# Kernel tuning notes

Hardware: AMD Instinct MI355X
Metric: run time of the kernel (lower is better)

The kernel has to match this reference:

```python
import jax, jax.numpy as jnp
import numpy as np

B, Nq, Nk, R = 4, 1024, 1024, 256
NH, DK, DV = 8, 64, 64


def setup_inputs() -> dict:
    key = jax.random.key(0)
    ks = jax.random.split(key, 16)
    mk = lambda k, shape, s=1.0: jax.random.normal(k, shape, dtype=jnp.float32) * s
    inp = {
        'Q_real': mk(ks[0], (B, Nq, R)), 'Q_imag': mk(ks[1], (B, Nq, R)),
        'K_real': mk(ks[2], (B, Nk, R)), 'K_imag': mk(ks[3], (B, Nk, R)),
        'V_real': mk(ks[4], (B, Nk, R)), 'V_imag': mk(ks[5], (B, Nk, R)),
        'WQ_r': mk(ks[6], (NH * DK, R), 0.02), 'WQ_i': mk(ks[7], (NH * DK, R), 0.02),
        'WK_r': mk(ks[8], (NH * DK, R), 0.02), 'WK_i': mk(ks[9], (NH * DK, R), 0.02),
        'WV_r': mk(ks[10], (NH * DV, R), 0.02), 'WV_i': mk(ks[11], (NH * DV, R), 0.02),
        'WO_r': mk(ks[12], (R, NH * DV), 0.02), 'WO_i': mk(ks[13], (R, NH * DV), 0.02),
        'mask': jax.random.randint(ks[14], (B, Nk), 0, 2).astype(bool),
    }
    return inp


def _complex_linear(x, w_r, w_i):
    # x: complex [..., in]; weights real [out, in]. Same math as 4 real matmuls.
    w = (w_r + 1j * w_i).astype(jnp.complex64)
    return x @ w.T


def reference(Q_real, Q_imag, K_real, K_imag, V_real, V_imag,
              WQ_r, WQ_i, WK_r, WK_i, WV_r, WV_i, WO_r, WO_i, mask):
    Q = (Q_real + 1j * Q_imag).astype(jnp.complex64)
    K = (K_real + 1j * K_imag).astype(jnp.complex64)
    V = (V_real + 1j * V_imag).astype(jnp.complex64)

    Qp = _complex_linear(Q, WQ_r, WQ_i).reshape(B, Nq, NH, DK).transpose(0, 2, 1, 3)
    Kp = _complex_linear(K, WK_r, WK_i).reshape(B, Nk, NH, DK).transpose(0, 2, 1, 3)
    Vp = _complex_linear(V, WV_r, WV_i).reshape(B, Nk, NH, DV).transpose(0, 2, 1, 3)

    # complex scores [B, NH, Nq, Nk]; conj on K matches torch .conj().transpose
    scores = jnp.einsum('bhqd,bhkd->bhqk', Qp, jnp.conj(Kp)) / jnp.sqrt(jnp.float32(DK))
    scores_abs = jnp.abs(scores)

    m = mask[:, None, None, :]                    # [B,1,1,Nk]
    valid = jnp.any(mask, axis=-1)[:, None, None, None]  # [B,1,1,1] valid query rows
    masked = jnp.where(m, scores_abs, -jnp.inf)
    # avoid all -inf rows feeding softmax (those rows are zeroed afterwards)
    safe = jnp.where(valid, masked, 0.0)
    w = jax.nn.softmax(safe, axis=-1)
    w = jnp.where(valid, w, 0.0)

    attn = jnp.einsum('bhqk,bhkd->bhqd', w.astype(Vp.dtype), Vp)
    attn = attn.transpose(0, 2, 1, 3).reshape(B, Nq, NH * DV)
    return _complex_linear(attn, WO_r, WO_i)
```

## Files before the change

kernel.cpp:

```cpp
#include <hip/hip_runtime.h>
#include <hip/hip_bf16.h>

#define NBATCH 4
#define NSEQ   1024
#define RD     256
#define NHEAD  8
#define HD     64
#define NHD    512

typedef __attribute__((ext_vector_type(8))) short  short8;
typedef __attribute__((ext_vector_type(4))) short  short4v;
typedef __attribute__((ext_vector_type(4))) float  float4v;

#define MFMA16(a,b,c) __builtin_amdgcn_mfma_f32_16x16x32_bf16(a,b,c,0,0,0)

typedef const void __attribute__((address_space(1)))* gas_t;
typedef void __attribute__((address_space(3)))* las_t;
#define GLOAD16(g, l) __builtin_amdgcn_global_load_lds((gas_t)(g), (las_t)(l), 16, 0, 0)

static __device__ __forceinline__ short f2b(float f) {
    __hip_bfloat16 h = __float2bfloat16(f);
    union { __hip_bfloat16 h; short s; } u; u.h = h;
    return u.s;
}
static __device__ __forceinline__ void st4(short* dst, float4v v) {
    short4v p;
    p[0] = f2b(v[0]); p[1] = f2b(v[1]);
    p[2] = f2b(v[2]); p[3] = f2b(v[3]);
    *(short4v*)dst = p;
}

struct ConvArgs { const float* src[15]; short* dst[15]; int n4[15]; };

__global__ __launch_bounds__(256) void convert_bf16(ConvArgs ca)
{
    const int a = blockIdx.y;
    if (a == 14) {
        if (blockIdx.x != 0) return;
        __shared__ int isByteLayout;
        const int t = threadIdx.x;
        if (t == 0) isByteLayout = 0;
        __syncthreads();
        const int* mi = (const int*)ca.src[14];
        #pragma unroll
        for (int j = 0; j < 4; j++) {
            int v = mi[t*4 + j];
            if (v & ~1) isByteLayout = 1;
        }
        __syncthreads();
        const unsigned char* mb = (const unsigned char*)ca.src[14];
        unsigned char mv[16];
        int lc = 0;
        if (isByteLayout) {
            #pragma unroll
            for (int j = 0; j < 16; j++) { mv[j] = mb[t*16 + j] ? 1 : 0; lc += mv[j]; }
        } else {
            #pragma unroll
            for (int j = 0; j < 16; j++) { mv[j] = mi[t*16 + j] ? 1 : 0; lc += mv[j]; }
        }
        const int lane = t & 63, b = t >> 6;
        int sum = lc;
        #pragma unroll
        for (int d = 1; d < 64; d <<= 1) {
            int o = __shfl_up(sum, d, 64);
            if (lane >= d) sum += o;
        }
        int p = sum - lc;
        unsigned short* idxOut = (unsigned short*)ca.dst[14];
        int* cntOut = (int*)(idxOut + 4096);
        unsigned short* ib = idxOut + b*1024;
        #pragma unroll
        for (int j = 0; j < 16; j++)
            if (mv[j]) ib[p++] = (unsigned short)(lane*16 + j);
        if (lane == 63) cntOut[b] = sum;
        return;
    }
    if (a >= 2 && a <= 5) {
        const int t = threadIdx.x;
        const int r0 = blockIdx.x * 16;
        const int b  = r0 >> 10;
        __shared__ int isByteLayout;
        __shared__ unsigned short ib[1024];
        __shared__ int scnt;
        if (t == 0) isByteLayout = 0;
        __syncthreads();
        const int* mi = (const int*)ca.src[14];
        #pragma unroll
        for (int j = 0; j < 4; j++) {
            int v = mi[t*4 + j];
            if (v & ~1) isByteLayout = 1;
        }
        __syncthreads();
        if (t < 64) {
            const unsigned char* mb8 = (const unsigned char*)ca.src[14];
            unsigned char mv[16]; int lc = 0;
            if (isByteLayout) {
                #pragma unroll
                for (int j = 0; j < 16; j++) { mv[j] = mb8[b*1024 + t*16 + j] ? 1 : 0; lc += mv[j]; }
            } else {
                #pragma unroll
                for (int j = 0; j < 16; j++) { mv[j] = mi[b*1024 + t*16 + j] ? 1 : 0; lc += mv[j]; }
            }
            int sum = lc;
            #pragma unroll
            for (int d = 1; d < 64; d <<= 1) {
                int o = __shfl_up(sum, d, 64);
                if (t >= d) sum += o;
            }
            int p = sum - lc;
            #pragma unroll
            for (int j = 0; j < 16; j++)
                if (mv[j]) ib[p++] = (unsigned short)(t*16 + j);
            if (t == 63) scnt = sum;
        }
        __syncthreads();
        const int cb = scnt, L = (cb + 63) & ~63;
        const float* __restrict__ s = ca.src[a];
        short* __restrict__ d = ca.dst[a];
        const int jj = t >> 4, c = t & 15;
        const int j  = r0 + jj;
        const int jl = j & 1023;
        if (jl < L) {
            short* dp = d + (size_t)j*RD + c*4;
            if (jl < cb) {
                const float* sp = s + ((size_t)(b*NSEQ) + ib[jl])*RD + c*4;
                #pragma unroll
                for (int u = 0; u < 4; u++) {
                    float4v v = *(const float4v*)(sp + u*64);
                    st4(dp + u*64, v);
                }
            } else {
                short4v z = {0,0,0,0};
                #pragma unroll
                for (int u = 0; u < 4; u++) *(short4v*)(dp + u*64) = z;
            }
        }
        return;
    }
    const float* __restrict__ s = ca.src[a];
    short* __restrict__ d = ca.dst[a];
    const int n4 = ca.n4[a];
    for (int i = blockIdx.x*256 + threadIdx.x; i < n4; i += gridDim.x*256) {
        float4v v = *(const float4v*)(s + (size_t)i*4);
        st4(d + (size_t)i*4, v);
    }
}

struct ProjArgs {
    const short* Xr[3]; const short* Xi[3];
    const short* Wr[3]; const short* Wi[3];
    short* Yr[3]; short* Yi[3];
    const int* cnt;
};

__global__ __launch_bounds__(256) void cgemm_proj(ProjArgs pa)
{
    __shared__ __align__(16) char smemP[49152];
    short (*sX)[2][128][32] = (short(*)[2][128][32])smemP;
    short (*sW)[2][64][32]  = (short(*)[2][64][32])(smemP + 32768);

    const int wgid = blockIdx.x;
    const int flat = (wgid & 7) * 96 + (wgid >> 3);
    const int nx = flat & 7, my = (flat >> 3) & 31, z = flat >> 8;
    const int n0 = nx * 64, m0 = my * 128;

    if (z >= 1) {
        int b  = m0 >> 10;
        int nb = m0 & 1023;
        int L  = (pa.cnt[b] + 63) & ~63;
        if (nb >= L) return;
    }
    const short* __restrict__ X_r = pa.Xr[z];
    const short* __restrict__ X_i = pa.Xi[z];
    const short* __restrict__ W_r = pa.Wr[z];
    const short* __restrict__ W_i = pa.Wi[z];
    short* __restrict__ Y_r = pa.Yr[z];
    short* __restrict__ Y_i = pa.Yi[z];
    const int transposeOut = (z == 2);

    const int tid  = threadIdx.x;
    const int lane = tid & 63, wave = tid >> 6;
    const int quad = lane >> 4, l16 = lane & 15;
    const int lrow = lane >> 2;
    const int scg  = (lane & 3) ^ (lrow & 3);

    const short nk = (short)0x8000;
    const short8 neg = {nk,nk,nk,nk,nk,nk,nk,nk};

    float4v zf = {0.f,0.f,0.f,0.f};
    float4v Yr[2][4], Yi[2][4];
    #pragma unroll
    for (int ms = 0; ms < 2; ms++)
        #pragma unroll
        for (int t = 0; t < 4; t++) { Yr[ms][t] = zf; Yi[ms][t] = zf; }

    #define PROJ_STAGE(kc, bf)                                                \
        if (wave < 2) {                                                       \
            const short* gp = wave ? X_i : X_r;                               \
            short* lp = &sX[bf][wave][0][0];                                  \
            _Pragma("unroll")                                                 \
            for (int j = 0; j < 8; j++)                                       \
                GLOAD16(gp + (size_t)(m0 + j*16 + lrow)*RD + (kc) + scg*8,    \
                        lp + j*512);                                          \
        } else {                                                              \
            const short* gp = (wave == 3) ? W_i : W_r;                        \
            short* lp = &sW[bf][wave - 2][0][0];                              \
            _Pragma("unroll")                                                 \
            for (int j = 0; j < 4; j++)                                       \
                GLOAD16(gp + (size_t)(n0 + j*16 + lrow)*RD + (kc) + scg*8,    \
                        lp + j*512);                                          \
        }

    PROJ_STAGE(0, 0);

    const int xsh = l16 & 3;
    for (int c = 0; c < 8; c++) {
        __syncthreads();
        if (c + 1 < 8) { PROJ_STAGE((c + 1)*32, (c + 1) & 1); }
        const int bf = c & 1;
        const int u = (quad ^ xsh) * 8;

        short8 fxr[2], fxi[2], fxin[2];
        #pragma unroll
        for (int ms = 0; ms < 2; ms++) {
            int row = wave*32 + ms*16 + l16;
            fxr[ms]  = *(short8*)&sX[bf][0][row][u];
            fxi[ms]  = *(short8*)&sX[bf][1][row][u];
            fxin[ms] = fxi[ms] ^ neg;
        }
        #pragma unroll
        for (int t = 0; t < 4; t++) {
            short8 wr = *(short8*)&sW[bf][0][t*16 + l16][u];
            short8 wi = *(short8*)&sW[bf][1][t*16 + l16][u];
            #pragma unroll
            for (int ms = 0; ms < 2; ms++) {
                Yr[ms][t] = MFMA16(fxr[ms],  wr, Yr[ms][t]);
                Yr[ms][t] = MFMA16(fxin[ms], wi, Yr[ms][t]);
                Yi[ms][t] = MFMA16(fxr[ms],  wi, Yi[ms][t]);
                Yi[ms][t] = MFMA16(fxi[ms],  wr, Yi[ms][t]);
            }
        }
    }
    #undef PROJ_STAGE

    const int b = m0 >> 10, h = n0 >> 6, nb = m0 & 1023;
    short* sT = (short*)smemP;
    const int PLSZ = transposeOut ? 8448 : 8704;
    __syncthreads();
    #pragma unroll
    for (int ms = 0; ms < 2; ms++)
        #pragma unroll
        for (int t = 0; t < 4; t++)
            #pragma unroll
            for (int r = 0; r < 4; r++) {
                int rr = wave*32 + ms*16 + quad*4 + r;
                int cc = t*16 + l16;
                if (!transposeOut) {
                    sT[rr*68 + cc]          = f2b(Yr[ms][t][r]);
                    sT[PLSZ + rr*68 + cc]   = f2b(Yi[ms][t][r]);
                } else {
                    sT[cc*132 + rr]         = f2b(Yr[ms][t][r]);
                    sT[PLSZ + cc*132 + rr]  = f2b(Yi[ms][t][r]);
                }
            }
    __syncthreads();
    short* Yp[2] = { Y_r, Y_i };
    #pragma unroll
    for (int p = 0; p < 2; p++) {
        #pragma unroll
        for (int it = 0; it < 4; it++) {
            int idx = it*256 + tid;
            int rr, c8;
            size_t o;
            const short* sp;
            if (!transposeOut) {
                rr = idx >> 3; c8 = (idx & 7)*8;
                sp = &sT[p*PLSZ + rr*68 + c8];
                o = (((size_t)(b*NHEAD + h))*NSEQ + nb + rr)*HD + c8;
            } else {
                rr = idx >> 4; c8 = (idx & 15)*8;
                sp = &sT[p*PLSZ + rr*132 + c8];
                o = (((size_t)(b*NHEAD + h))*HD + rr)*NSEQ + nb + c8;
            }
            short4v a = *(short4v*)sp;
            short4v bq = *(short4v*)(sp + 4);
            short8 v8 = { a[0],a[1],a[2],a[3], bq[0],bq[1],bq[2],bq[3] };
            *(short8*)&Yp[p][o] = v8;
        }
    }
}

__global__ __launch_bounds__(512) void attn_mfma(
    const short* __restrict__ Qp_r, const short* __restrict__ Qp_i,
    const short* __restrict__ Kp_r, const short* __restrict__ Kp_i,
    const short* __restrict__ Vp_r, const short* __restrict__ Vp_i,
    const int* __restrict__ cnt,
    short* __restrict__ Ar, short* __restrict__ Ai)
{
    __shared__ __align__(16) char smem[75776];
    short (*sP)[16][40] = (short(*)[16][40])(smem + 65536);

    const int tid  = threadIdx.x;
    const int lane = tid & 63, wave = tid >> 6;
    const int quad = lane >> 4, l16 = lane & 15;
    const int sw8  = l16 & 7;
    const int qstrip = wave >> 1;
    const int khalf  = wave & 1;
    const int qt = blockIdx.x >> 5;
    const int bh = blockIdx.x & 31;
    const int b  = bh >> 3, h = bh & 7;
    const size_t base = (size_t)bh * (NSEQ*HD);

    const int rsub = lane >> 3;
    const int colg = (lane & 7) ^ rsub;

    const int cb = cnt[b];
    const int nt = (cb + 63) >> 6;

    const int splane = wave >> 1;
    const short* sgp = (splane == 0) ? Kp_r : (splane == 1) ? Kp_i
                     : (splane == 2) ? Vp_r : Vp_i;
    const int sisV = (splane >= 2);
    const int soff = splane * 8192;

    const short nk = (short)0x8000;
    const short8 neg = {nk,nk,nk,nk,nk,nk,nk,nk};
    short8 fqr[2], fqi[2], fqrn[2];
    #pragma unroll
    for (int ds = 0; ds < 2; ds++) {
        size_t qo = base + (size_t)(qt*64 + qstrip*16 + l16)*HD + ds*32 + quad*8;
        fqr[ds]  = *(const short8*)&Qp_r[qo];
        fqi[ds]  = *(const short8*)&Qp_i[qo];
        fqrn[ds] = fqr[ds] ^ neg;
    }

    float4v zf = {0.f,0.f,0.f,0.f};
    float4v Or[4], Oi[4];
    float lrow[4];
    #pragma unroll
    for (int t = 0; t < 4; t++) { Or[t] = zf; Oi[t] = zf; }
    #pragma unroll
    for (int r = 0; r < 4; r++) lrow[r] = 0.f;

    const float C2 = 0.18033688f;

    if (nt > 0) {
        short* lp = (short*)(smem + soff);
        #pragma unroll
        for (int jj = 0; jj < 4; jj++) {
            int j = (wave & 1)*4 + jj;
            int row = j*8 + rsub;
            const short* g = sisV
                ? sgp + base + (size_t)row*NSEQ + colg*8
                : sgp + base + (size_t)row*HD + colg*8;
            GLOAD16(g, lp + j*512);
        }
    }

    for (int kt = 0; kt < nt; kt++) {
        __syncthreads();

        if (kt + 1 < nt) {
            const int kn = (kt + 1) * 64;
            short* lp = (short*)(smem + ((kt + 1) & 1)*32768 + soff);
            #pragma unroll
            for (int jj = 0; jj < 4; jj++) {
                int j = (wave & 1)*4 + jj;
                int row = j*8 + rsub;
                const short* g = sisV
                    ? sgp + base + (size_t)row*NSEQ + kn + colg*8
                    : sgp + base + (size_t)(kn + row)*HD + colg*8;
                GLOAD16(g, lp + j*512);
            }
        }

        const char* buf = smem + (kt & 1)*32768;
        short (*sK0)[64] = (short(*)[64])(buf);
        short (*sK1)[64] = (short(*)[64])(buf + 8192);
        short (*sV0)[64] = (short(*)[64])(buf + 16384);
        short (*sV1)[64] = (short(*)[64])(buf + 24576);
        const int k0 = kt*64;

        float4v Sr[2], Si[2];
        Sr[0] = zf; Sr[1] = zf; Si[0] = zf; Si[1] = zf;
        __builtin_amdgcn_s_setprio(1);
        #pragma unroll
        for (int t = 0; t < 2; t++)
            #pragma unroll
            for (int ds = 0; ds < 2; ds++) {
                int u = ((ds*4 + quad) ^ sw8) * 8;
                int krow = khalf*32 + t*16 + l16;
                short8 kr = *(short8*)&sK0[krow][u];
                short8 ki = *(short8*)&sK1[krow][u];
                Sr[t] = MFMA16(fqr[ds],  kr, Sr[t]);
                Sr[t] = MFMA16(fqi[ds],  ki, Sr[t]);
                Si[t] = MFMA16(fqi[ds],  kr, Si[t]);
                Si[t] = MFMA16(fqrn[ds], ki, Si[t]);
            }
        __builtin_amdgcn_s_setprio(0);

        #pragma unroll
        for (int t = 0; t < 2; t++) {
            bool mv = (k0 + khalf*32 + t*16 + l16) < cb;
            #pragma unroll
            for (int r = 0; r < 4; r++) {
                float a = Sr[t][r], c = Si[t][r];
                float x = fmaf(a, a, c*c);
                float s = __builtin_amdgcn_sqrtf(x);
                float e = mv ? __builtin_amdgcn_exp2f(C2 * s) : 0.f;
                lrow[r] += e;
                sP[wave][quad*4 + r][t*16 + l16] = f2b(e);
            }
        }

        {
            short8 fp = *(short8*)&sP[wave][l16][quad*8];
            __builtin_amdgcn_s_setprio(1);
            #pragma unroll
            for (int t = 0; t < 4; t++) {
                int u = ((khalf*4 + quad) ^ sw8) * 8;
                short8 vr = *(short8*)&sV0[t*16 + l16][u];
                short8 vi = *(short8*)&sV1[t*16 + l16][u];
                Or[t] = MFMA16(fp, vr, Or[t]);
                Oi[t] = MFMA16(fp, vi, Oi[t]);
            }
            __builtin_amdgcn_s_setprio(0);
        }
    }

    __syncthreads();
    float* sC = (float*)smem;
    float* sL = (float*)(smem + 32768);
    if (khalf == 1) {
        #pragma unroll
        for (int t = 0; t < 4; t++)
            #pragma unroll
            for (int r = 0; r < 4; r++) {
                int o8 = ((qstrip*4 + t)*64 + lane)*8 + r*2;
                sC[o8]     = Or[t][r];
                sC[o8 + 1] = Oi[t][r];
            }
        int lo = (qstrip*64 + lane)*4;
        #pragma unroll
        for (int r = 0; r < 4; r++) sL[lo + r] = lrow[r];
    }
    __syncthreads();
    if (khalf == 0) {
        #pragma unroll
        for (int t = 0; t < 4; t++)
            #pragma unroll
            for (int r = 0; r < 4; r++) {
                int o8 = ((qstrip*4 + t)*64 + lane)*8 + r*2;
                Or[t][r] += sC[o8];
                Oi[t][r] += sC[o8 + 1];
            }
        int lo = (qstrip*64 + lane)*4;
        float inv[4];
        #pragma unroll
        for (int r = 0; r < 4; r++) {
            float ls = lrow[r] + sL[lo + r];
            ls += __shfl_xor(ls, 1, 64);
            ls += __shfl_xor(ls, 2, 64);
            ls += __shfl_xor(ls, 4, 64);
            ls += __shfl_xor(ls, 8, 64);
            inv[r] = (ls > 0.f) ? 1.f/ls : 0.f;
        }
        #pragma unroll
        for (int t = 0; t < 4; t++)
            #pragma unroll
            for (int r = 0; r < 4; r++) {
                int q = qt*64 + qstrip*16 + quad*4 + r;
                int d = t*16 + l16;
                size_t o = ((size_t)(b*NSEQ + q))*NHD + h*HD + d;
                Ar[o] = f2b(Or[t][r] * inv[r]);
                Ai[o] = f2b(Oi[t][r] * inv[r]);
            }
    }
}

__global__ __launch_bounds__(256) void cgemm_out(
    const short* __restrict__ A_r, const short* __restrict__ A_i,
    const short* __restrict__ W_r, const short* __restrict__ W_i,
    float* __restrict__ Out, int writeImagPlane)
{
    __shared__ short sA[2][2][64][64];
    __shared__ short sW[2][2][32][64];
    const int tid  = threadIdx.x;
    const int lane = tid & 63, wave = tid >> 6;
    const int quad = lane >> 4, l16 = lane & 15;
    const int sw8  = l16 & 7;
    const int rsub = lane >> 3;
    const int colg = (lane & 7) ^ rsub;

    const int wgid = blockIdx.x;
    const int flat = (wgid & 7) * 64 + (wgid >> 3);
    const int n0 = (flat & 7) * 32, m0 = (flat >> 3) * 64;

    const short nk = (short)0x8000;
    const short8 neg = {nk,nk,nk,nk,nk,nk,nk,nk};

    float4v zf = {0.f,0.f,0.f,0.f};
    float4v Yr[2], Yi[2];
    #pragma unroll
    for (int t = 0; t < 2; t++) { Yr[t] = zf; Yi[t] = zf; }

    #define OUT_STAGE(kc, bf)                                                 \
        if (wave < 2) {                                                       \
            const short* gp = wave ? A_i : A_r;                               \
            short* lp = &sA[bf][wave][0][0];                                  \
            _Pragma("unroll")                                                 \
            for (int j = 0; j < 8; j++)                                       \
                GLOAD16(gp + (size_t)(m0 + j*8 + rsub)*NHD + (kc) + colg*8,   \
                        lp + j*512);                                          \
        } else {                                                              \
            const short* gp = (wave == 3) ? W_i : W_r;                        \
            short* lp = &sW[bf][wave - 2][0][0];                              \
            _Pragma("unroll")                                                 \
            for (int j = 0; j < 4; j++)                                       \
                GLOAD16(gp + (size_t)(n0 + j*8 + rsub)*NHD + (kc) + colg*8,   \
                        lp + j*512);                                          \
        }

    OUT_STAGE(0, 0);

    for (int c = 0; c < 8; c++) {
        __syncthreads();
        if (c + 1 < 8) { OUT_STAGE((c + 1)*64, (c + 1) & 1); }
        const int bf = c & 1;

        short8 far[2], fai[2], fain[2];
        #pragma unroll
        for (int ds = 0; ds < 2; ds++) {
            int u = ((ds*4 + quad) ^ sw8) * 8;
            far[ds]  = *(short8*)&sA[bf][0][wave*16 + l16][u];
            fai[ds]  = *(short8*)&sA[bf][1][wave*16 + l16][u];
            fain[ds] = fai[ds] ^ neg;
        }
        #pragma unroll
        for (int t = 0; t < 2; t++)
            #pragma unroll
            for (int ds = 0; ds < 2; ds++) {
                int u = ((ds*4 + quad) ^ sw8) * 8;
                short8 wr = *(short8*)&sW[bf][0][t*16 + l16][u];
                short8 wi = *(short8*)&sW[bf][1][t*16 + l16][u];
                Yr[t] = MFMA16(far[ds],  wr, Yr[t]);
                Yr[t] = MFMA16(fain[ds], wi, Yr[t]);
                Yi[t] = MFMA16(far[ds],  wi, Yi[t]);
                Yi[t] = MFMA16(fai[ds],  wr, Yi[t]);
            }
    }
    #undef OUT_STAGE

    const size_t TOT = (size_t)NBATCH * NSEQ * RD;
    #pragma unroll
    for (int t = 0; t < 2; t++)
        #pragma unroll
        for (int r = 0; r < 4; r++) {
            int row = m0 + wave*16 + quad*4 + r;
            int col = n0 + t*16 + l16;
            size_t o = (size_t)row*RD + col;
            Out[o] = Yr[t][r];
            if (writeImagPlane) Out[o + TOT] = Yi[t][r];
        }
}

extern "C" void kernel_launch(void* const* d_in, const int* in_sizes, int n_in,
                              void* d_out, int out_size, void* d_ws, size_t ws_size,
                              hipStream_t stream)
{
    float* out = (float*)d_out;

    const size_t P = (size_t)NBATCH * NHEAD * NSEQ * HD;
    const size_t H = (size_t)NBATCH * NSEQ * RD;
    const size_t WSZ = (size_t)NHD * RD;

    short* bws = (short*)d_ws;
    short* Qpr = bws + 0*P;  short* Qpi = bws + 1*P;
    short* Kpr = bws + 2*P;  short* Kpi = bws + 3*P;
    short* Vpr = bws + 4*P;  short* Vpi = bws + 5*P;
    short* conv = bws + 6*P;
    short* cX[6]; for (int i = 0; i < 6; i++) cX[i] = conv + i*H;
    short* cW[6]; for (int i = 0; i < 6; i++) cW[i] = conv + 6*H + i*WSZ;
    short* cWOr = conv + 6*H + 6*WSZ;
    short* cWOi = conv + 6*H + 7*WSZ;
    unsigned short* midx = (unsigned short*)(conv + 6*H + 8*WSZ);
    int* mcnt = (int*)(midx + 4096);
    short* Apr = conv;
    short* Api = conv + P;

    const size_t TOT = (size_t)NBATCH * NSEQ * RD;
    const int writeImagPlane = ((size_t)out_size >= 2*TOT) ? 1 : 0;

    ConvArgs ca;
    for (int i = 0; i < 6; i++) {
        ca.src[i] = (const float*)d_in[i];  ca.dst[i] = cX[i];  ca.n4[i] = (int)(H/4);
    }
    for (int i = 0; i < 6; i++) {
        ca.src[6+i] = (const float*)d_in[6+i]; ca.dst[6+i] = cW[i]; ca.n4[6+i] = (int)(WSZ/4);
    }
    ca.src[12] = (const float*)d_in[12]; ca.dst[12] = cWOr; ca.n4[12] = (int)(WSZ/4);
    ca.src[13] = (const float*)d_in[13]; ca.dst[13] = cWOi; ca.n4[13] = (int)(WSZ/4);
    ca.src[14] = (const float*)d_in[14]; ca.dst[14] = (short*)midx; ca.n4[14] = 0;

    ProjArgs pa;
    pa.Xr[0] = cX[0]; pa.Xi[0] = cX[1];
    pa.Xr[1] = cX[2]; pa.Xi[1] = cX[3];
    pa.Xr[2] = cX[4]; pa.Xi[2] = cX[5];
    pa.Wr[0] = cW[0]; pa.Wi[0] = cW[1];
    pa.Wr[1] = cW[2]; pa.Wi[1] = cW[3];
    pa.Wr[2] = cW[4]; pa.Wi[2] = cW[5];
    pa.Yr[0] = Qpr; pa.Yi[0] = Qpi;
    pa.Yr[1] = Kpr; pa.Yi[1] = Kpi;
    pa.Yr[2] = Vpr; pa.Yi[2] = Vpi;
    pa.cnt = mcnt;

    convert_bf16<<<dim3(256, 15), 256, 0, stream>>>(ca);
    cgemm_proj<<<dim3(768), 256, 0, stream>>>(pa);
    attn_mfma<<<dim3(512), 512, 0, stream>>>(Qpr, Qpi, Kpr, Kpi, Vpr, Vpi,
                                             mcnt, Apr, Api);
    cgemm_out<<<dim3(512), 256, 0, stream>>>(Apr, Api, cWOr, cWOi, out,
                                             writeImagPlane);
}
```

Measured before the change: 147.5 us.

## Fuse fp32-to-bf16 conversion into projection and output GEMM tile loads

Drops the separate conversion kernel. The projection and output GEMMs now read fp32 inputs and weights directly, convert them to bf16 in registers, and write them to LDS, with the masked-row gather for K/V moved into the projection load path. A small mask-scan kernel is kept to build the index lists. This removes a full write and re-read of bf16 copies of the activations and weights. In exchange the GEMMs use register-staged loads instead of asynchronous global-to-LDS loads, which adds register pressure and conversion ALU work, and each weight element is converted repeatedly across tiles.

```diff
diff --git a/kernel.cpp b/kernel.cpp
--- a/kernel.cpp
+++ b/kernel.cpp
@@ -23,134 +23,52 @@
     union { __hip_bfloat16 h; short s; } u; u.h = h;
     return u.s;
 }
-static __device__ __forceinline__ void st4(short* dst, float4v v) {
-    short4v p;
-    p[0] = f2b(v[0]); p[1] = f2b(v[1]);
-    p[2] = f2b(v[2]); p[3] = f2b(v[3]);
-    *(short4v*)dst = p;
+
+__global__ __launch_bounds__(256) void mask_scan(
+    const void* __restrict__ msrc, unsigned short* __restrict__ midx,
+    int* __restrict__ mcnt)
+{
+    __shared__ int isByteLayout;
+    const int t = threadIdx.x;
+    if (t == 0) isByteLayout = 0;
+    __syncthreads();
+    const int* mi = (const int*)msrc;
+    #pragma unroll
+    for (int j = 0; j < 4; j++) {
+        int v = mi[t*4 + j];
+        if (v & ~1) isByteLayout = 1;
+    }
+    __syncthreads();
+    const unsigned char* mb = (const unsigned char*)msrc;
+    unsigned char mv[16];
+    int lc = 0;
+    if (isByteLayout) {
+        #pragma unroll
+        for (int j = 0; j < 16; j++) { mv[j] = mb[t*16 + j] ? 1 : 0; lc += mv[j]; }
+    } else {
+        #pragma unroll
+        for (int j = 0; j < 16; j++) { mv[j] = mi[t*16 + j] ? 1 : 0; lc += mv[j]; }
+    }
+    const int lane = t & 63, b = t >> 6;
+    int sum = lc;
+    #pragma unroll
+    for (int d = 1; d < 64; d <<= 1) {
+        int o = __shfl_up(sum, d, 64);
+        if (lane >= d) sum += o;
+    }
+    int p = sum - lc;
+    unsigned short* ib = midx + b*1024;
+    #pragma unroll
+    for (int j = 0; j < 16; j++)
+        if (mv[j]) ib[p++] = (unsigned short)(lane*16 + j);
+    if (lane == 63) mcnt[b] = sum;
 }
 
-struct ConvArgs { const float* src[15]; short* dst[15]; int n4[15]; };
-
-__global__ __launch_bounds__(256) void convert_bf16(ConvArgs ca)
-{
-    const int a = blockIdx.y;
-    if (a == 14) {
-        if (blockIdx.x != 0) return;
-        __shared__ int isByteLayout;
-        const int t = threadIdx.x;
-        if (t == 0) isByteLayout = 0;
-        __syncthreads();
-        const int* mi = (const int*)ca.src[14];
-        #pragma unroll
-        for (int j = 0; j < 4; j++) {
-            int v = mi[t*4 + j];
-            if (v & ~1) isByteLayout = 1;
-        }
-        __syncthreads();
-        const unsigned char* mb = (const unsigned char*)ca.src[14];
-        unsigned char mv[16];
-        int lc = 0;
-        if (isByteLayout) {
-            #pragma unroll
-            for (int j = 0; j < 16; j++) { mv[j] = mb[t*16 + j] ? 1 : 0; lc += mv[j]; }
-        } else {
-            #pragma unroll
-            for (int j = 0; j < 16; j++) { mv[j] = mi[t*16 + j] ? 1 : 0; lc += mv[j]; }
-        }
-        const int lane = t & 63, b = t >> 6;
-        int sum = lc;
-        #pragma unroll
-        for (int d = 1; d < 64; d <<= 1) {
-            int o = __shfl_up(sum, d, 64);
-            if (lane >= d) sum += o;
-        }
-        int p = sum - lc;
-        unsigned short* idxOut = (unsigned short*)ca.dst[14];
-        int* cntOut = (int*)(idxOut + 4096);
-        unsigned short* ib = idxOut + b*1024;
-        #pragma unroll
-        for (int j = 0; j < 16; j++)
-            if (mv[j]) ib[p++] = (unsigned short)(lane*16 + j);
-        if (lane == 63) cntOut[b] = sum;
-        return;
-    }
-    if (a >= 2 && a <= 5) {
-        const int t = threadIdx.x;
-        const int r0 = blockIdx.x * 16;
-        const int b  = r0 >> 10;
-        __shared__ int isByteLayout;
-        __shared__ unsigned short ib[1024];
-        __shared__ int scnt;
-        if (t == 0) isByteLayout = 0;
-        __syncthreads();
-        const int* mi = (const int*)ca.src[14];
-        #pragma unroll
-        for (int j = 0; j < 4; j++) {
-            int v = mi[t*4 + j];
-            if (v & ~1) isByteLayout = 1;
-        }
-        __syncthreads();
-        if (t < 64) {
-            const unsigned char* mb8 = (const unsigned char*)ca.src[14];
-            unsigned char mv[16]; int lc = 0;
-            if (isByteLayout) {
-                #pragma unroll
-                for (int j = 0; j < 16; j++) { mv[j] = mb8[b*1024 + t*16 + j] ? 1 : 0; lc += mv[j]; }
-            } else {
-                #pragma unroll
-                for (int j = 0; j < 16; j++) { mv[j] = mi[b*1024 + t*16 + j] ? 1 : 0; lc += mv[j]; }
-            }
-            int sum = lc;
-            #pragma unroll
-            for (int d = 1; d < 64; d <<= 1) {
-                int o = __shfl_up(sum, d, 64);
-                if (t >= d) sum += o;
-            }
-            int p = sum - lc;
-            #pragma unroll
-            for (int j = 0; j < 16; j++)
-                if (mv[j]) ib[p++] = (unsigned short)(t*16 + j);
-            if (t == 63) scnt = sum;
-        }
-        __syncthreads();
-        const int cb = scnt, L = (cb + 63) & ~63;
-        const float* __restrict__ s = ca.src[a];
-        short* __restrict__ d = ca.dst[a];
-        const int jj = t >> 4, c = t & 15;
-        const int j  = r0 + jj;
-        const int jl = j & 1023;
-        if (jl < L) {
-            short* dp = d + (size_t)j*RD + c*4;
-            if (jl < cb) {
-                const float* sp = s + ((size_t)(b*NSEQ) + ib[jl])*RD + c*4;
-                #pragma unroll
-                for (int u = 0; u < 4; u++) {
-                    float4v v = *(const float4v*)(sp + u*64);
-                    st4(dp + u*64, v);
-                }
-            } else {
-                short4v z = {0,0,0,0};
-                #pragma unroll
-                for (int u = 0; u < 4; u++) *(short4v*)(dp + u*64) = z;
-            }
-        }
-        return;
-    }
-    const float* __restrict__ s = ca.src[a];
-    short* __restrict__ d = ca.dst[a];
-    const int n4 = ca.n4[a];
-    for (int i = blockIdx.x*256 + threadIdx.x; i < n4; i += gridDim.x*256) {
-        float4v v = *(const float4v*)(s + (size_t)i*4);
-        st4(d + (size_t)i*4, v);
-    }
-}
-
 struct ProjArgs {
-    const short* Xr[3]; const short* Xi[3];
-    const short* Wr[3]; const short* Wi[3];
+    const float* Xr[3]; const float* Xi[3];
+    const float* Wr[3]; const float* Wi[3];
     short* Yr[3]; short* Yi[3];
-    const int* cnt;
+    const unsigned short* idx; const int* cnt;
 };
 
 __global__ __launch_bounds__(256) void cgemm_proj(ProjArgs pa)
@@ -163,17 +81,17 @@
     const int flat = (wgid & 7) * 96 + (wgid >> 3);
     const int nx = flat & 7, my = (flat >> 3) & 31, z = flat >> 8;
     const int n0 = nx * 64, m0 = my * 128;
+    const int b = m0 >> 10;
 
     if (z >= 1) {
-        int b  = m0 >> 10;
         int nb = m0 & 1023;
         int L  = (pa.cnt[b] + 63) & ~63;
         if (nb >= L) return;
     }
-    const short* __restrict__ X_r = pa.Xr[z];
-    const short* __restrict__ X_i = pa.Xi[z];
-    const short* __restrict__ W_r = pa.Wr[z];
-    const short* __restrict__ W_i = pa.Wi[z];
+    const float* __restrict__ X_r = pa.Xr[z];
+    const float* __restrict__ X_i = pa.Xi[z];
+    const float* __restrict__ W_r = pa.Wr[z];
+    const float* __restrict__ W_i = pa.Wi[z];
     short* __restrict__ Y_r = pa.Yr[z];
     short* __restrict__ Y_i = pa.Yi[z];
     const int transposeOut = (z == 2);
@@ -181,8 +99,32 @@
     const int tid  = threadIdx.x;
     const int lane = tid & 63, wave = tid >> 6;
     const int quad = lane >> 4, l16 = lane & 15;
-    const int lrow = lane >> 2;
-    const int scg  = (lane & 3) ^ (lrow & 3);
+    const int row_l = lane >> 2;
+    const int cg    = lane & 3;
+
+    const int ncell = (wave < 2) ? 8 : 4;
+    const float* SP = (wave < 2) ? (wave ? X_i : X_r)
+                                 : ((wave == 3) ? W_i : W_r);
+    const int cb = (z >= 1) ? pa.cnt[b] : NSEQ;
+    const float* rp[8];
+    int rvm = 0;
+    #pragma unroll
+    for (int cl = 0; cl < 8; cl++) {
+        if (cl < ncell) {
+            int row = cl*16 + row_l;
+            int colg = ((cg ^ (row & 3)) * 8);
+            if (wave < 2) {
+                if (z == 0) { rp[cl] = SP + (size_t)(m0 + row)*RD + colg; rvm |= 1 << cl; }
+                else {
+                    int jl = (m0 & 1023) + row;
+                    if (jl < cb) {
+                        rp[cl] = SP + ((size_t)b*NSEQ + pa.idx[b*NSEQ + jl])*RD + colg;
+                        rvm |= 1 << cl;
+                    } else rp[cl] = SP + colg;
+                }
+            } else { rp[cl] = SP + (size_t)(n0 + row)*RD + colg; rvm |= 1 << cl; }
+        }
+    }
 
     const short nk = (short)0x8000;
     const short8 neg = {nk,nk,nk,nk,nk,nk,nk,nk};
@@ -194,29 +136,35 @@
         #pragma unroll
         for (int t = 0; t < 4; t++) { Yr[ms][t] = zf; Yi[ms][t] = zf; }
 
-    #define PROJ_STAGE(kc, bf)                                                \
-        if (wave < 2) {                                                       \
-            const short* gp = wave ? X_i : X_r;                               \
-            short* lp = &sX[bf][wave][0][0];                                  \
-            _Pragma("unroll")                                                 \
-            for (int j = 0; j < 8; j++)                                       \
-                GLOAD16(gp + (size_t)(m0 + j*16 + lrow)*RD + (kc) + scg*8,    \
-                        lp + j*512);                                          \
-        } else {                                                              \
-            const short* gp = (wave == 3) ? W_i : W_r;                        \
-            short* lp = &sW[bf][wave - 2][0][0];                              \
-            _Pragma("unroll")                                                 \
-            for (int j = 0; j < 4; j++)                                       \
-                GLOAD16(gp + (size_t)(n0 + j*16 + lrow)*RD + (kc) + scg*8,    \
-                        lp + j*512);                                          \
-        }
-
-    PROJ_STAGE(0, 0);
+    float4v ta[8], tb[8];
+    #define PROJ_LOAD(kc)                                                     \
+        _Pragma("unroll")                                                     \
+        for (int cl = 0; cl < 8; cl++) if (cl < ncell) {                      \
+            ta[cl] = *(const float4v*)(rp[cl] + (kc));                        \
+            tb[cl] = *(const float4v*)(rp[cl] + (kc) + 4);                    \
+        }
+    #define PROJ_WRITE(bf)                                                    \
+        _Pragma("unroll")                                                     \
+        for (int cl = 0; cl < 8; cl++) if (cl < ncell) {                      \
+            short8 s;                                                         \
+            if (rvm & (1 << cl)) {                                            \
+                s[0]=f2b(ta[cl][0]); s[1]=f2b(ta[cl][1]);                     \
+                s[2]=f2b(ta[cl][2]); s[3]=f2b(ta[cl][3]);                     \
+                s[4]=f2b(tb[cl][0]); s[5]=f2b(tb[cl][1]);                     \
+                s[6]=f2b(tb[cl][2]); s[7]=f2b(tb[cl][3]);                     \
+            } else { s = short8{0,0,0,0,0,0,0,0}; }                           \
+            short* dst = (wave < 2)                                           \
+                ? &sX[bf][wave][cl*16 + row_l][cg*8]                          \
+                : &sW[bf][wave - 2][cl*16 + row_l][cg*8];                     \
+            *(short8*)dst = s;                                                \
+        }
+
+    PROJ_LOAD(0); PROJ_WRITE(0);
 
     const int xsh = l16 & 3;
     for (int c = 0; c < 8; c++) {
         __syncthreads();
-        if (c + 1 < 8) { PROJ_STAGE((c + 1)*32, (c + 1) & 1); }
+        if (c < 7) { PROJ_LOAD((c + 1)*32); }
         const int bf = c & 1;
         const int u = (quad ^ xsh) * 8;
 
@@ -240,10 +188,12 @@
                 Yi[ms][t] = MFMA16(fxi[ms],  wr, Yi[ms][t]);
             }
         }
-    }
-    #undef PROJ_STAGE
-
-    const int b = m0 >> 10, h = n0 >> 6, nb = m0 & 1023;
+        if (c < 7) { PROJ_WRITE((c + 1) & 1); }
+    }
+    #undef PROJ_LOAD
+    #undef PROJ_WRITE
+
+    const int h = n0 >> 6, nb = m0 & 1023;
     short* sT = (short*)smemP;
     const int PLSZ = transposeOut ? 8448 : 8704;
     __syncthreads();
@@ -480,7 +430,7 @@
 
 __global__ __launch_bounds__(256) void cgemm_out(
     const short* __restrict__ A_r, const short* __restrict__ A_i,
-    const short* __restrict__ W_r, const short* __restrict__ W_i,
+    const float* __restrict__ Wf_r, const float* __restrict__ Wf_i,
     float* __restrict__ Out, int writeImagPlane)
 {
     __shared__ short sA[2][2][64][64];
@@ -504,28 +454,48 @@
     #pragma unroll
     for (int t = 0; t < 2; t++) { Yr[t] = zf; Yi[t] = zf; }
 
-    #define OUT_STAGE(kc, bf)                                                 \
-        if (wave < 2) {                                                       \
+    const float* Wfp = (wave == 3) ? Wf_i : Wf_r;
+    const float* rp[4];
+    #pragma unroll
+    for (int cl = 0; cl < 4; cl++)
+        rp[cl] = Wfp + (size_t)(n0 + cl*8 + rsub)*NHD + colg*8;
+
+    float4v ta[4], tb[4];
+    #define OUT_ALOAD(kc, bf)                                                 \
+        {                                                                     \
             const short* gp = wave ? A_i : A_r;                               \
             short* lp = &sA[bf][wave][0][0];                                  \
             _Pragma("unroll")                                                 \
             for (int j = 0; j < 8; j++)                                       \
                 GLOAD16(gp + (size_t)(m0 + j*8 + rsub)*NHD + (kc) + colg*8,   \
                         lp + j*512);                                          \
-        } else {                                                              \
-            const short* gp = (wave == 3) ? W_i : W_r;                        \
-            short* lp = &sW[bf][wave - 2][0][0];                              \
-            _Pragma("unroll")                                                 \
-            for (int j = 0; j < 4; j++)                                       \
-                GLOAD16(gp + (size_t)(n0 + j*8 + rsub)*NHD + (kc) + colg*8,   \
-                        lp + j*512);                                          \
-        }
-
-    OUT_STAGE(0, 0);
+        }
+    #define OUT_WLOAD(kc)                                                     \
+        _Pragma("unroll")                                                     \
+        for (int cl = 0; cl < 4; cl++) {                                      \
+            ta[cl] = *(const float4v*)(rp[cl] + (kc));                        \
+            tb[cl] = *(const float4v*)(rp[cl] + (kc) + 4);                    \
+        }
+    #define OUT_WWRITE(bf)                                                    \
+        _Pragma("unroll")                                                     \
+        for (int cl = 0; cl < 4; cl++) {                                      \
+            short8 s;                                                         \
+            s[0]=f2b(ta[cl][0]); s[1]=f2b(ta[cl][1]);                         \
+            s[2]=f2b(ta[cl][2]); s[3]=f2b(ta[cl][3]);                         \
+            s[4]=f2b(tb[cl][0]); s[5]=f2b(tb[cl][1]);                         \
+            s[6]=f2b(tb[cl][2]); s[7]=f2b(tb[cl][3]);                         \
+            *(short8*)&sW[bf][wave - 2][cl*8 + rsub][(lane & 7)*8] = s;       \
+        }
+
+    if (wave < 2) { OUT_ALOAD(0, 0); }
+    else          { OUT_WLOAD(0); OUT_WWRITE(0); }
 
     for (int c = 0; c < 8; c++) {
         __syncthreads();
-        if (c + 1 < 8) { OUT_STAGE((c + 1)*64, (c + 1) & 1); }
+        if (c < 7) {
+            if (wave < 2) { OUT_ALOAD((c + 1)*64, (c + 1) & 1); }
+            else          { OUT_WLOAD((c + 1)*64); }
+        }
         const int bf = c & 1;
 
         short8 far[2], fai[2], fain[2];
@@ -548,8 +518,11 @@
                 Yi[t] = MFMA16(far[ds],  wi, Yi[t]);
                 Yi[t] = MFMA16(fai[ds],  wr, Yi[t]);
             }
-    }
-    #undef OUT_STAGE
+        if (c < 7 && wave >= 2) { OUT_WWRITE((c + 1) & 1); }
+    }
+    #undef OUT_ALOAD
+    #undef OUT_WLOAD
+    #undef OUT_WWRITE
 
     const size_t TOT = (size_t)NBATCH * NSEQ * RD;
     #pragma unroll
@@ -579,45 +552,32 @@
     short* Kpr = bws + 2*P;  short* Kpi = bws + 3*P;
     short* Vpr = bws + 4*P;  short* Vpi = bws + 5*P;
     short* conv = bws + 6*P;
-    short* cX[6]; for (int i = 0; i < 6; i++) cX[i] = conv + i*H;
-    short* cW[6]; for (int i = 0; i < 6; i++) cW[i] = conv + 6*H + i*WSZ;
-    short* cWOr = conv + 6*H + 6*WSZ;
-    short* cWOi = conv + 6*H + 7*WSZ;
+    short* Apr = conv;
+    short* Api = conv + P;
     unsigned short* midx = (unsigned short*)(conv + 6*H + 8*WSZ);
     int* mcnt = (int*)(midx + 4096);
-    short* Apr = conv;
-    short* Api = conv + P;
 
     const size_t TOT = (size_t)NBATCH * NSEQ * RD;
     const int writeImagPlane = ((size_t)out_size >= 2*TOT) ? 1 : 0;
 
-    ConvArgs ca;
-    for (int i = 0; i < 6; i++) {
-        ca.src[i] = (const float*)d_in[i];  ca.dst[i] = cX[i];  ca.n4[i] = (int)(H/4);
-    }
-    for (int i = 0; i < 6; i++) {
-        ca.src[6+i] = (const float*)d_in[6+i]; ca.dst[6+i] = cW[i]; ca.n4[6+i] = (int)(WSZ/4);
-    }
-    ca.src[12] = (const float*)d_in[12]; ca.dst[12] = cWOr; ca.n4[12] = (int)(WSZ/4);
-    ca.src[13] = (const float*)d_in[13]; ca.dst[13] = cWOi; ca.n4[13] = (int)(WSZ/4);
-    ca.src[14] = (const float*)d_in[14]; ca.dst[14] = (short*)midx; ca.n4[14] = 0;
-
     ProjArgs pa;
-    pa.Xr[0] = cX[0]; pa.Xi[0] = cX[1];
-    pa.Xr[1] = cX[2]; pa.Xi[1] = cX[3];
-    pa.Xr[2] = cX[4]; pa.Xi[2] = cX[5];
-    pa.Wr[0] = cW[0]; pa.Wi[0] = cW[1];
-    pa.Wr[1] = cW[2]; pa.Wi[1] = cW[3];
-    pa.Wr[2] = cW[4]; pa.Wi[2] = cW[5];
+    pa.Xr[0] = (const float*)d_in[0];  pa.Xi[0] = (const float*)d_in[1];
+    pa.Xr[1] = (const float*)d_in[2];  pa.Xi[1] = (const float*)d_in[3];
+    pa.Xr[2] = (const float*)d_in[4];  pa.Xi[2] = (const float*)d_in[5];
+    pa.Wr[0] = (const float*)d_in[6];  pa.Wi[0] = (const float*)d_in[7];
+    pa.Wr[1] = (const float*)d_in[8];  pa.Wi[1] = (const float*)d_in[9];
+    pa.Wr[2] = (const float*)d_in[10]; pa.Wi[2] = (const float*)d_in[11];
     pa.Yr[0] = Qpr; pa.Yi[0] = Qpi;
     pa.Yr[1] = Kpr; pa.Yi[1] = Kpi;
     pa.Yr[2] = Vpr; pa.Yi[2] = Vpi;
-    pa.cnt = mcnt;
-
-    convert_bf16<<<dim3(256, 15), 256, 0, stream>>>(ca);
+    pa.idx = midx; pa.cnt = mcnt;
+
+    mask_scan<<<dim3(1), 256, 0, stream>>>(d_in[14], midx, mcnt);
     cgemm_proj<<<dim3(768), 256, 0, stream>>>(pa);
     attn_mfma<<<dim3(512), 512, 0, stream>>>(Qpr, Qpi, Kpr, Kpi, Vpr, Vpi,
                                              mcnt, Apr, Api);
-    cgemm_out<<<dim3(512), 256, 0, stream>>>(Apr, Api, cWOr, cWOi, out,
-                                             writeImagPlane);
+    cgemm_out<<<dim3(512), 256, 0, stream>>>(Apr, Api,
+                                             (const float*)d_in[12],
+                                             (const float*)d_in[13],
+                                             out, writeImagPlane);
 }
```

Measured after the change: 158.0 us. +7.2%, slower.

## Triple-buffer LDS staging with explicit vmcnt waits in projection and output GEMMs

Applied to the files above, without the earlier changes.

Both complex GEMM kernels move from double to triple LDS buffering, issuing global-to-LDS loads two chunks ahead. The loops are fully unrolled and use per-wave s_waitcnt vmcnt counts plus a raw s_barrier instead of __syncthreads. This lets loads overlap more with MFMA work and avoids a full memory drain at every barrier. The cost is more shared memory per block (72KB in the projection kernel), which may lower occupancy, and the barrier-free reuse of buffers depends on the wait counts being correct.

```diff
diff --git a/kernel.cpp b/kernel.cpp
--- a/kernel.cpp
+++ b/kernel.cpp
@@ -155,9 +155,8 @@
 
 __global__ __launch_bounds__(256) void cgemm_proj(ProjArgs pa)
 {
-    __shared__ __align__(16) char smemP[49152];
-    short (*sX)[2][128][32] = (short(*)[2][128][32])smemP;
-    short (*sW)[2][64][32]  = (short(*)[2][64][32])(smemP + 32768);
+    __shared__ short sX[3][2][128][32];
+    __shared__ short sW[3][2][64][32];
 
     const int wgid = blockIdx.x;
     const int flat = (wgid & 7) * 96 + (wgid >> 3);
@@ -194,6 +193,8 @@
         #pragma unroll
         for (int t = 0; t < 4; t++) { Yr[ms][t] = zf; Yi[ms][t] = zf; }
 
+    const int xsh = l16 & 3;
+
     #define PROJ_STAGE(kc, bf)                                                \
         if (wave < 2) {                                                       \
             const short* gp = wave ? X_i : X_r;                               \
@@ -211,40 +212,58 @@
                         lp + j*512);                                          \
         }
 
+    #define PROJ_MFMA(bfc)                                                    \
+        {                                                                     \
+            const int bf = (bfc);                                             \
+            const int u = (quad ^ xsh) * 8;                                   \
+            short8 fxr[2], fxi[2], fxin[2];                                   \
+            _Pragma("unroll")                                                 \
+            for (int ms = 0; ms < 2; ms++) {                                  \
+                int row = wave*32 + ms*16 + l16;                              \
+                fxr[ms]  = *(short8*)&sX[bf][0][row][u];                      \
+                fxi[ms]  = *(short8*)&sX[bf][1][row][u];                      \
+                fxin[ms] = fxi[ms] ^ neg;                                     \
+            }                                                                 \
+            _Pragma("unroll")                                                 \
+            for (int t = 0; t < 4; t++) {                                     \
+                short8 wr = *(short8*)&sW[bf][0][t*16 + l16][u];              \
+                short8 wi = *(short8*)&sW[bf][1][t*16 + l16][u];              \
+                _Pragma("unroll")                                             \
+                for (int ms = 0; ms < 2; ms++) {                              \
+                    Yr[ms][t] = MFMA16(fxr[ms],  wr, Yr[ms][t]);              \
+                    Yr[ms][t] = MFMA16(fxin[ms], wi, Yr[ms][t]);    \
+                    Yi[ms][t] = MFMA16(fxr[ms],  wi, Yi[ms][t]);              \
+                    Yi[ms][t] = MFMA16(fxi[ms],  wr, Yi[ms][t]);              \
+                }                                                             \
+            }                                                                 \
+        }
+
+    #define PROJ_CHUNK(c, NX, NW)                                             \
+        {                                                                     \
+            if (wave < 2) { asm volatile("s_waitcnt vmcnt(" #NX ")" ::: "memory"); } \
+            else          { asm volatile("s_waitcnt vmcnt(" #NW ")" ::: "memory"); } \
+            __builtin_amdgcn_s_barrier();                                     \
+            asm volatile("" ::: "memory");                                    \
+            if ((c) + 2 < 8) { PROJ_STAGE(((c) + 2)*32, ((c) + 2) % 3); }     \
+            PROJ_MFMA((c) % 3);                                               \
+        }
+
     PROJ_STAGE(0, 0);
-
-    const int xsh = l16 & 3;
-    for (int c = 0; c < 8; c++) {
-        __syncthreads();
-        if (c + 1 < 8) { PROJ_STAGE((c + 1)*32, (c + 1) & 1); }
-        const int bf = c & 1;
-        const int u = (quad ^ xsh) * 8;
-
-        short8 fxr[2], fxi[2], fxin[2];
-        #pragma unroll
-        for (int ms = 0; ms < 2; ms++) {
-            int row = wave*32 + ms*16 + l16;
-            fxr[ms]  = *(short8*)&sX[bf][0][row][u];
-            fxi[ms]  = *(short8*)&sX[bf][1][row][u];
-            fxin[ms] = fxi[ms] ^ neg;
-        }
-        #pragma unroll
-        for (int t = 0; t < 4; t++) {
-            short8 wr = *(short8*)&sW[bf][0][t*16 + l16][u];
-            short8 wi = *(short8*)&sW[bf][1][t*16 + l16][u];
-            #pragma unroll
-            for (int ms = 0; ms < 2; ms++) {
-                Yr[ms][t] = MFMA16(fxr[ms],  wr, Yr[ms][t]);
-                Yr[ms][t] = MFMA16(fxin[ms], wi, Yr[ms][t]);
-                Yi[ms][t] = MFMA16(fxr[ms],  wi, Yi[ms][t]);
-                Yi[ms][t] = MFMA16(fxi[ms],  wr, Yi[ms][t]);
-            }
-        }
-    }
+    PROJ_STAGE(32, 1);
+    PROJ_CHUNK(0, 8, 4)
+    PROJ_CHUNK(1, 8, 4)
+    PROJ_CHUNK(2, 8, 4)
+    PROJ_CHUNK(3, 8, 4)
+    PROJ_CHUNK(4, 8, 4)
+    PROJ_CHUNK(5, 8, 4)
+    PROJ_CHUNK(6, 8, 4)
+    PROJ_CHUNK(7, 0, 0)
+    #undef PROJ_CHUNK
+    #undef PROJ_MFMA
     #undef PROJ_STAGE
 
     const int b = m0 >> 10, h = n0 >> 6, nb = m0 & 1023;
-    short* sT = (short*)smemP;
+    short* sT = &sX[0][0][0][0];
     const int PLSZ = transposeOut ? 8448 : 8704;
     __syncthreads();
     #pragma unroll
@@ -483,8 +502,8 @@
     const short* __restrict__ W_r, const short* __restrict__ W_i,
     float* __restrict__ Out, int writeImagPlane)
 {
-    __shared__ short sA[2][2][64][64];
-    __shared__ short sW[2][2][32][64];
+    __shared__ short sA[3][2][64][64];
+    __shared__ short sW[3][2][32][64];
     const int tid  = threadIdx.x;
     const int lane = tid & 63, wave = tid >> 6;
     const int quad = lane >> 4, l16 = lane & 15;
@@ -521,34 +540,53 @@
                         lp + j*512);                                          \
         }
 
+    #define OUT_MFMA(bfc)                                                     \
+        {                                                                     \
+            const int bf = (bfc);                                             \
+            short8 far[2], fai[2], fain[2];                                   \
+            _Pragma("unroll")                                                 \
+            for (int ds = 0; ds < 2; ds++) {                                  \
+                int u = ((ds*4 + quad) ^ sw8) * 8;                            \
+                far[ds]  = *(short8*)&sA[bf][0][wave*16 + l16][u];            \
+                fai[ds]  = *(short8*)&sA[bf][1][wave*16 + l16][u];            \
+                fain[ds] = fai[ds] ^ neg;                                     \
+            }                                                                 \
+            _Pragma("unroll")                                                 \
+            for (int t = 0; t < 2; t++)                                       \
+                _Pragma("unroll")                                             \
+                for (int ds = 0; ds < 2; ds++) {                              \
+                    int u = ((ds*4 + quad) ^ sw8) * 8;                        \
+                    short8 wr = *(short8*)&sW[bf][0][t*16 + l16][u];          \
+                    short8 wi = *(short8*)&sW[bf][1][t*16 + l16][u];          \
+                    Yr[t] = MFMA16(far[ds],  wr, Yr[t]);                      \
+                    Yr[t] = MFMA16(fain[ds], wi, Yr[t]);                      \
+                    Yi[t] = MFMA16(far[ds],  wi, Yi[t]);                      \
+                    Yi[t] = MFMA16(fai[ds],  wr, Yi[t]);                      \
+                }                                                             \
+        }
+
+    #define OUT_CHUNK(c, NA, NW)                                              \
+        {                                                                     \
+            if (wave < 2) { asm volatile("s_waitcnt vmcnt(" #NA ")" ::: "memory"); } \
+            else          { asm volatile("s_waitcnt vmcnt(" #NW ")" ::: "memory"); } \
+            __builtin_amdgcn_s_barrier();                                     \
+            asm volatile("" ::: "memory");                                    \
+            if ((c) + 2 < 8) { OUT_STAGE(((c) + 2)*64, ((c) + 2) % 3); }      \
+            OUT_MFMA((c) % 3);                                                \
+        }
+
     OUT_STAGE(0, 0);
-
-    for (int c = 0; c < 8; c++) {
-        __syncthreads();
-        if (c + 1 < 8) { OUT_STAGE((c + 1)*64, (c + 1) & 1); }
-        const int bf = c & 1;
-
-        short8 far[2], fai[2], fain[2];
-        #pragma unroll
-        for (int ds = 0; ds < 2; ds++) {
-            int u = ((ds*4 + quad) ^ sw8) * 8;
-            far[ds]  = *(short8*)&sA[bf][0][wave*16 + l16][u];
-            fai[ds]  = *(short8*)&sA[bf][1][wave*16 + l16][u];
-            fain[ds] = fai[ds] ^ neg;
-        }
-        #pragma unroll
-        for (int t = 0; t < 2; t++)
-            #pragma unroll
-            for (int ds = 0; ds < 2; ds++) {
-                int u = ((ds*4 + quad) ^ sw8) * 8;
-                short8 wr = *(short8*)&sW[bf][0][t*16 + l16][u];
-                short8 wi = *(short8*)&sW[bf][1][t*16 + l16][u];
-                Yr[t] = MFMA16(far[ds],  wr, Yr[t]);
-                Yr[t] = MFMA16(fain[ds], wi, Yr[t]);
-                Yi[t] = MFMA16(far[ds],  wi, Yi[t]);
-                Yi[t] = MFMA16(fai[ds],  wr, Yi[t]);
-            }
-    }
+    OUT_STAGE(64, 1);
+    OUT_CHUNK(0, 8, 4)
+    OUT_CHUNK(1, 8, 4)
+    OUT_CHUNK(2, 8, 4)
+    OUT_CHUNK(3, 8, 4)
+    OUT_CHUNK(4, 8, 4)
+    OUT_CHUNK(5, 8, 4)
+    OUT_CHUNK(6, 8, 4)
+    OUT_CHUNK(7, 0, 0)
+    #undef OUT_CHUNK
+    #undef OUT_MFMA
     #undef OUT_STAGE
 
     const size_t TOT = (size_t)NBATCH * NSEQ * RD;
```

Measured after the change: 148.8 us. No clear change (+0.9%).
